# Optimization experiments

Measured on AMD Instinct MI355X. Metric: run time of the kernel, lower is better.

Reference implementation:

```python
import jax, jax.numpy as jnp
import numpy as np
from jax import lax

BOS = 0
B, T, U = 8, 256, 64
IN, ENC_H, DEC_H, P, J, V = 80, 512, 512, 512, 512, 1024


def lstm_layer(x, Wih, Whh, b):
    """PyTorch-style LSTM layer. x: [B,T,I]; Wih: [4H,I]; Whh: [4H,H]; b: [4H]."""
    Bn = x.shape[0]
    H = Whh.shape[1]
    xp = jnp.einsum('bti,gi->btg', x, Wih) + b  # precompute input projections [B,T,4H]
    h0 = jnp.zeros((Bn, H), x.dtype)

    def step(carry, xt):
        h, c = carry
        g = xt + h @ Whh.T
        i, f, gg, o = jnp.split(g, 4, axis=-1)
        c = jax.nn.sigmoid(f) * c + jax.nn.sigmoid(i) * jnp.tanh(gg)
        h = jax.nn.sigmoid(o) * jnp.tanh(c)
        return (h, c), h

    _, hs = lax.scan(step, (h0, h0), xp.transpose(1, 0, 2))
    return hs.transpose(1, 0, 2)  # [B,T,H]


def setup_inputs() -> dict:
    key = jax.random.key(0)
    ks = jax.random.split(key, 20)
    s = 0.04  # ~1/sqrt(H) init scale
    inp = {
        'xs': jax.random.normal(ks[0], (B, T, IN), jnp.float32),
        'ys': jax.random.randint(ks[1], (B, U), 0, V),
        # encoder LSTM layer 0 / 1
        'enc_Wih0': jax.random.normal(ks[2], (4 * ENC_H, IN), jnp.float32) * s,
        'enc_Whh0': jax.random.normal(ks[3], (4 * ENC_H, ENC_H), jnp.float32) * s,
        'enc_b0': jnp.zeros((4 * ENC_H,), jnp.float32),
        'enc_Wih1': jax.random.normal(ks[4], (4 * ENC_H, ENC_H), jnp.float32) * s,
        'enc_Whh1': jax.random.normal(ks[5], (4 * ENC_H, ENC_H), jnp.float32) * s,
        'enc_b1': jnp.zeros((4 * ENC_H,), jnp.float32),
        'enc_projW': jax.random.normal(ks[6], (P, ENC_H), jnp.float32) * s,
        'enc_projb': jnp.zeros((P,), jnp.float32),
        # decoder
        'embed': jax.random.normal(ks[7], (V, DEC_H), jnp.float32) * s,
        'dec_Wih': jax.random.normal(ks[8], (4 * DEC_H, DEC_H), jnp.float32) * s,
        'dec_Whh': jax.random.normal(ks[9], (4 * DEC_H, DEC_H), jnp.float32) * s,
        'dec_b': jnp.zeros((4 * DEC_H,), jnp.float32),
        'dec_projW': jax.random.normal(ks[10], (P, DEC_H), jnp.float32) * s,
        'dec_projb': jnp.zeros((P,), jnp.float32),
        # joint MLP: Linear(2P -> J), Tanh, Linear(J -> V)
        'jW1': jax.random.normal(ks[11], (J, 2 * P), jnp.float32) * s,
        'jb1': jnp.zeros((J,), jnp.float32),
        'jW2': jax.random.normal(ks[12], (V, J), jnp.float32) * s,
        'jb2': jnp.zeros((V,), jnp.float32),
    }
    return inp


def reference(xs, ys, enc_Wih0, enc_Whh0, enc_b0, enc_Wih1, enc_Whh1, enc_b1,
              enc_projW, enc_projb, embed, dec_Wih, dec_Whh, dec_b,
              dec_projW, dec_projb, jW1, jb1, jW2, jb2):
    # Encoder: 2-layer LSTM + projection
    h = lstm_layer(xs, enc_Wih0, enc_Whh0, enc_b0)
    h = lstm_layer(h, enc_Wih1, enc_Whh1, enc_b1)
    h_enc = h @ enc_projW.T + enc_projb  # [B,T,P]

    # Decoder: BOS pad, embed, 1-layer LSTM + projection
    ys_p = jnp.pad(ys, ((0, 0), (1, 0)), constant_values=BOS)  # [B,U+1]
    e = embed[ys_p]
    hd = lstm_layer(e, dec_Wih, dec_Whh, dec_b)
    h_dec = hd @ dec_projW.T + dec_projb  # [B,U+1,P]

    # Joint: cat([h_enc,h_dec]) @ W1.T == h_enc @ W1[:,:P].T + h_dec @ W1[:,P:].T
    pre_enc = jnp.einsum('btp,jp->btj', h_enc, jW1[:, :P])
    pre_dec = jnp.einsum('bup,jp->buj', h_dec, jW1[:, P:])
    z = jnp.tanh(pre_enc[:, :, None, :] + pre_dec[:, None, :, :] + jb1)  # [B,T,U+1,J]
    logits = jnp.einsum('btuj,vj->btuv', z, jW2) + jb2  # [B,T,U+1,V]
    return logits
```

## Files before the change

kernel.cpp:

```cpp
#include <hip/hip_runtime.h>


typedef _Float16 f16;
typedef _Float16 f16x8 __attribute__((ext_vector_type(8)));
typedef float f32x4 __attribute__((ext_vector_type(4)));
using u32 = unsigned int;

#define BB   8
#define TT   256
#define UU1  65
#define HH   512
#define G4   2048
#define JJ   512
#define VV   1024
#define SENT 0xFFFFFFFFu

#define LOADX(p)     __hip_atomic_load((p), __ATOMIC_RELAXED, __HIP_MEMORY_SCOPE_AGENT)
#define STOREX(p, v) __hip_atomic_store((p), (v), __ATOMIC_RELAXED, __HIP_MEMORY_SCOPE_AGENT)

static __device__ __forceinline__ u32 packf16(float a, float b) {
  f16 ha = (f16)a, hb = (f16)b;
  unsigned short ua = __builtin_bit_cast(unsigned short, ha);
  unsigned short ub = __builtin_bit_cast(unsigned short, hb);
  return (u32)ua | ((u32)ub << 16);
}
static __device__ __forceinline__ float sigm(float x) {
  x = fminf(30.f, fmaxf(-30.f, x));
  return __builtin_amdgcn_rcpf(1.f + __expf(-x));
}
static __device__ __forceinline__ float ftanh(float x) {
  x = fminf(15.f, fmaxf(-15.f, x));
  float t = __expf(2.f * x);
  return (t - 1.f) * __builtin_amdgcn_rcpf(t + 1.f);
}

__global__ void k_init(u32* __restrict__ p, int n, int z1, int z2, int zt) {
  int i = blockIdx.x * 256 + threadIdx.x;
  if (i >= n) return;
  bool z = (i < 2048) | ((u32)(i - z1) < 2048u) | ((u32)(i - z2) < 2048u) | (i >= zt);
  p[i] = z ? 0u : SENT;
}

struct CastSeg { const float* s; f16* d; int n4; };
struct CastArgs { CastSeg seg[10]; };
__global__ void k_cast_all(CastArgs a, int total4) {
  int i = blockIdx.x * 256 + threadIdx.x;
  if (i >= total4) return;
  int k = 0, off = i;
  while (off >= a.seg[k].n4) { off -= a.seg[k].n4; ++k; }
  const float4 v = *(const float4*)(a.seg[k].s + (size_t)off * 4);
  uint2 p; p.x = packf16(v.x, v.y); p.y = packf16(v.z, v.w);
  *(uint2*)(a.seg[k].d + (size_t)off * 4) = p;
}

__global__ void k_embed(const int* __restrict__ ys, const float* __restrict__ emb,
                        float* __restrict__ e) {
  int row = blockIdx.x;
  int b = row / UU1, u = row % UU1;
  int idx = (u == 0) ? 0 : ys[b * (UU1 - 1) + (u - 1)];
  const float4* s = (const float4*)(emb + (size_t)idx * HH);
  float4* d = (float4*)(e + (size_t)row * HH);
  d[threadIdx.x] = s[threadIdx.x];
}

__global__ void k_biasdot(const float* __restrict__ jW1, const float* __restrict__ encPb,
                          const float* __restrict__ dPb, const float* __restrict__ jb1,
                          float* __restrict__ bce, float* __restrict__ bcd) {
  int j = blockIdx.x * 256 + threadIdx.x;
  if (j >= 512) return;
  const float* rowE = jW1 + (size_t)j * 1024;
  const float* rowD = rowE + 512;
  float s1 = 0.f, s2 = 0.f;
  for (int p = 0; p < 512; p += 4) {
    float4 a = *(const float4*)(rowE + p), b = *(const float4*)(encPb + p);
    s1 += a.x * b.x + a.y * b.y + a.z * b.z + a.w * b.w;
    float4 c = *(const float4*)(rowD + p), d = *(const float4*)(dPb + p);
    s2 += c.x * d.x + c.y * d.y + c.z * d.z + c.w * d.w;
  }
  bce[j] = s1; bcd[j] = s2 + jb1[j];
}

__global__ __launch_bounds__(256) void k_gemm(
    const float* __restrict__ A, const f16* __restrict__ B,
    const float* __restrict__ bias, float* __restrict__ C,
    int M, int N, int K, int lda, int ldb) {
  __shared__ f16 As[128][72];
  __shared__ f16 Bs[128][72];
  int tid = threadIdx.x;
  int mb = blockIdx.y * 128, nb = blockIdx.x * 128;
  int wave = tid >> 6, lane = tid & 63;
  int wm = wave >> 1, wn = wave & 1;
  int rowa = lane & 15, kg = lane >> 4;
  f32x4 acc[4][4] = {};
  for (int k0 = 0; k0 < K; k0 += 64) {
    for (int idx = tid; idx < 2048; idx += 256) {
      int r = idx >> 4, cq = idx & 15;
      int gm = mb + r, gk = k0 + cq * 4;
      float4 v = make_float4(0.f, 0.f, 0.f, 0.f);
      if (gm < M && gk + 3 < K) v = *(const float4*)(A + (size_t)gm * lda + gk);
      uint2 p; p.x = packf16(v.x, v.y); p.y = packf16(v.z, v.w);
      *(uint2*)&As[r][cq * 4] = p;
    }
    for (int idx = tid; idx < 1024; idx += 256) {
      int r = idx >> 3, c8 = idx & 7;
      int gn = nb + r, gk = k0 + c8 * 8;
      uint4 v = make_uint4(0u, 0u, 0u, 0u);
      if (gn < N && gk + 7 < K) v = *(const uint4*)(B + (size_t)gn * ldb + gk);
      *(uint4*)&Bs[r][c8 * 8] = v;
    }
    __syncthreads();
#pragma unroll
    for (int kf = 0; kf < 2; ++kf) {
      f16x8 af[4], bf[4];
#pragma unroll
      for (int mt = 0; mt < 4; ++mt)
        af[mt] = *(const f16x8*)&As[wm * 64 + mt * 16 + rowa][kf * 32 + kg * 8];
#pragma unroll
      for (int nt = 0; nt < 4; ++nt)
        bf[nt] = *(const f16x8*)&Bs[wn * 64 + nt * 16 + rowa][kf * 32 + kg * 8];
#pragma unroll
      for (int mt = 0; mt < 4; ++mt)
#pragma unroll
        for (int nt = 0; nt < 4; ++nt)
          acc[mt][nt] = __builtin_amdgcn_mfma_f32_16x16x32_f16(af[mt], bf[nt], acc[mt][nt], 0, 0, 0);
    }
    __syncthreads();
  }
#pragma unroll
  for (int nt = 0; nt < 4; ++nt) {
    int gn = nb + wn * 64 + nt * 16 + rowa;
    float bv = bias ? bias[gn] : 0.f;
#pragma unroll
    for (int mt = 0; mt < 4; ++mt)
#pragma unroll
      for (int r = 0; r < 4; ++r) {
        int gm = mb + wm * 64 + mt * 16 + kg * 4 + r;
        if (gm < M) C[(size_t)gm * N + gn] = acc[mt][nt][r] + bv;
      }
  }
}

__global__ __launch_bounds__(256) void k_gemmT(
    const float* __restrict__ A, int lda, const f16* __restrict__ B2,
    f16* __restrict__ C16) {
  __shared__ f16 As[128][72];
  __shared__ f16 Bs[128][72];
  int tid = threadIdx.x;
  int mb = blockIdx.y * 128, nb = blockIdx.x * 128;
  int wave = tid >> 6, lane = tid & 63;
  int wm = wave >> 1, wn = wave & 1;
  int rowa = lane & 15, kg = lane >> 4;
  f32x4 acc[4][4] = {};
  for (int k0 = 0; k0 < 512; k0 += 64) {
    for (int idx = tid; idx < 2048; idx += 256) {
      int r = idx >> 4, cq = idx & 15;
      float4 v = *(const float4*)(A + (size_t)(mb + r) * lda + k0 + cq * 4);
      uint2 p; p.x = packf16(v.x, v.y); p.y = packf16(v.z, v.w);
      *(uint2*)&As[r][cq * 4] = p;
    }
    for (int idx = tid; idx < 1024; idx += 256) {
      int r = idx >> 4, c8 = idx & 15;
      uint4 v = *(const uint4*)(B2 + (size_t)(k0 + r) * 512 + nb + c8 * 8);
      f16 tmp[8]; *(uint4*)tmp = v;
#pragma unroll
      for (int e = 0; e < 8; ++e) Bs[c8 * 8 + e][r] = tmp[e];
    }
    __syncthreads();
#pragma unroll
    for (int kf = 0; kf < 2; ++kf) {
      f16x8 af[4], bf[4];
#pragma unroll
      for (int mt = 0; mt < 4; ++mt)
        af[mt] = *(const f16x8*)&As[wm * 64 + mt * 16 + rowa][kf * 32 + kg * 8];
#pragma unroll
      for (int nt = 0; nt < 4; ++nt)
        bf[nt] = *(const f16x8*)&Bs[wn * 64 + nt * 16 + rowa][kf * 32 + kg * 8];
#pragma unroll
      for (int mt = 0; mt < 4; ++mt)
#pragma unroll
        for (int nt = 0; nt < 4; ++nt)
          acc[mt][nt] = __builtin_amdgcn_mfma_f32_16x16x32_f16(af[mt], bf[nt], acc[mt][nt], 0, 0, 0);
    }
    __syncthreads();
  }
#pragma unroll
  for (int nt = 0; nt < 4; ++nt) {
    int gn = nb + wn * 64 + nt * 16 + rowa;
#pragma unroll
    for (int mt = 0; mt < 4; ++mt)
#pragma unroll
      for (int r = 0; r < 4; ++r) {
        int gm = mb + wm * 64 + mt * 16 + kg * 4 + r;
        C16[(size_t)gm * 512 + gn] = (f16)acc[mt][nt][r];
      }
  }
}

template <int NW>
static __device__ __forceinline__ void poll_batch(const u32* const* p, u32* vv) {
#pragma unroll
  for (int k = 0; k < NW; ++k) vv[k] = LOADX(p[k]);
  int gd = 0;
  while (++gd < (1 << 18)) {
    bool any = false;
#pragma unroll
    for (int k = 0; k < NW; ++k) any = any | (vv[k] == SENT);
    if (!any) break;
    __builtin_amdgcn_s_sleep(4);
#pragma unroll
    for (int k = 0; k < NW; ++k)
      if (vv[k] == SENT) vv[k] = LOADX(p[k]);
  }
}
static __device__ __forceinline__ void guard_spin(const u32* gp) {
  u32 v = LOADX(gp);
  int gd = 0;
  while (v == SENT && ++gd < (1 << 18)) {
    __builtin_amdgcn_s_sleep(1);
    v = LOADX(gp);
  }
}
static __device__ __forceinline__ void prog_spin(const u32* fp) {
  u32 v = LOADX(fp);
  int gd = 0;
  while (v < 8u && ++gd < (1 << 18)) {
    __builtin_amdgcn_s_sleep(8);
    v = LOADX(fp);
  }
}

static __device__ __forceinline__ void lstm_16(
    int wg, const float* __restrict__ xp, const f16* __restrict__ Whh,
    u32* __restrict__ hseq, int S) {
  extern __shared__ char smem[];
  f16 (*W)[520] = (f16(*)[520])smem;
  f16 (*H)[520] = (f16(*)[520])(smem + 133120);
  float (*gat)[8][36] = (float(*)[8][36])(smem + 133120 + 8320);
  const int tid = threadIdx.x;
  const int u0 = wg * 32;
  const int wave = tid >> 6, lane = tid & 63;
  const int rowa = lane & 15, kg = lane >> 4;
  const int b = lane >> 3, ju = lane & 7;
  const int uglob = u0 + wave * 8 + ju;

  for (int idx = tid; idx < 128 * 64; idx += 256) {
    int r = idx >> 6, ck = idx & 63;
    int w = r >> 5, g = (r >> 3) & 3, u = r & 7;
    uint4 v = *(const uint4*)(Whh + ((size_t)(g * 512 + u0 + w * 8 + u)) * 512 + ck * 8);
    *(uint4*)&W[r][ck * 8] = v;
  }
  __syncthreads();

  float c = 0.f;
  for (int t = 0; t < S; ++t) {
    const u32* hb = hseq + (size_t)t * 2048;
    if (tid < 16) guard_spin(hb + tid * 16);
    __syncthreads();

    size_t xpo = ((size_t)b * S + t) * (size_t)G4 + uglob;
    float xi = xp[xpo], xf = xp[xpo + 512], xg = xp[xpo + 1024], xo = xp[xpo + 1536];

    const u32* ptr[8];
    u32 vv[8];
#pragma unroll
    for (int k = 0; k < 8; ++k) ptr[k] = hb + ((tid + k * 256) >> 8) * 256 + ((tid + k * 256) & 255);
    poll_batch<8>(ptr, vv);
#pragma unroll
    for (int k = 0; k < 8; ++k) {
      int idx = tid + k * 256;
      ((u32*)H)[(idx >> 8) * 260 + (idx & 255)] = vv[k];
    }
    __syncthreads();

    f32x4 acc0 = {0.f, 0.f, 0.f, 0.f}, acc1 = {0.f, 0.f, 0.f, 0.f};
#pragma unroll
    for (int kf = 0; kf < 16; ++kf) {
      f16x8 af = {};
      if (rowa < 8) af = *(const f16x8*)&H[rowa][kf * 32 + kg * 8];
      f16x8 b0 = *(const f16x8*)&W[wave * 32 + rowa][kf * 32 + kg * 8];
      f16x8 b1 = *(const f16x8*)&W[wave * 32 + 16 + rowa][kf * 32 + kg * 8];
      acc0 = __builtin_amdgcn_mfma_f32_16x16x32_f16(af, b0, acc0, 0, 0, 0);
      acc1 = __builtin_amdgcn_mfma_f32_16x16x32_f16(af, b1, acc1, 0, 0, 0);
    }
    if (kg < 2) {
#pragma unroll
      for (int r = 0; r < 4; ++r) {
        gat[wave][kg * 4 + r][rowa] = acc0[r];
        gat[wave][kg * 4 + r][16 + rowa] = acc1[r];
      }
    }
    float gi = gat[wave][b][ju] + xi;
    float gf = gat[wave][b][8 + ju] + xf;
    float gg = gat[wave][b][16 + ju] + xg;
    float go = gat[wave][b][24 + ju] + xo;
    c = sigm(gf) * c + sigm(gi) * ftanh(gg);
    float h = sigm(go) * ftanh(c);

    float hn = __shfl_down(h, 1);
    if ((ju & 1) == 0)
      STOREX(hseq + (size_t)(t + 1) * 2048 + ((b * 512 + uglob) >> 1), packf16(h, hn));
  }
}

static __device__ __forceinline__ void lstm_l1(
    int wg, const float* __restrict__ gb, const f16* __restrict__ Wih,
    const f16* __restrict__ Whh, const u32* __restrict__ hin,
    u32* __restrict__ hseq, int S) {
  extern __shared__ char smem[];
  f16 (*W)[1032] = (f16(*)[1032])smem;
  f16 (*H)[1032] = (f16(*)[1032])(smem + 132096);
  float (*gat)[8][20] = (float(*)[8][20])(smem + 132096 + 16512);
  const int tid = threadIdx.x;
  const int u0 = wg * 16;
  const int wave = tid >> 6, lane = tid & 63;
  const int rowa = lane & 15, kg = lane >> 4;
  const int b = lane >> 2, ju = lane & 3;
  const int uglob = u0 + wave * 4 + ju;

  for (int idx = tid; idx < 64 * 64; idx += 256) {
    int r = idx >> 6, ck = idx & 63;
    int w = r >> 4, g = (r >> 2) & 3, u = r & 3;
    size_t grow = (size_t)(g * 512 + u0 + w * 4 + u) * 512;
    *(uint4*)&W[r][ck * 8]       = *(const uint4*)(Whh + grow + ck * 8);
    *(uint4*)&W[r][512 + ck * 8] = *(const uint4*)(Wih + grow + ck * 8);
  }
  float gbi = 0.f, gbf = 0.f, gbg = 0.f, gbo = 0.f;
  if (lane < 32) {
    gbi = gb[uglob]; gbf = gb[512 + uglob];
    gbg = gb[1024 + uglob]; gbo = gb[1536 + uglob];
  }
  __syncthreads();

  float c = 0.f;
  for (int t = 0; t < S; ++t) {
    const u32* hbS = hseq + (size_t)t * 2048;
    const u32* hbU = hin + (size_t)(t + 1) * 2048;
    if (tid < 32)       guard_spin(hbS + tid * 8);
    else if (tid < 48)  guard_spin(hbU + (tid - 32) * 16);
    __syncthreads();
    const u32* ptr[16];
    u32 vv[16];
#pragma unroll
    for (int k = 0; k < 8; ++k) {
      int idx = tid + k * 256;
      int r = idx >> 8, cu = idx & 255;
      ptr[k] = hbS + r * 256 + cu;
      ptr[k + 8] = hbU + r * 256 + cu;
    }
    poll_batch<16>(ptr, vv);
#pragma unroll
    for (int k = 0; k < 8; ++k) {
      int idx = tid + k * 256;
      int r = idx >> 8, cu = idx & 255;
      ((u32*)H)[r * 516 + cu] = vv[k];
      ((u32*)H)[r * 516 + 256 + cu] = vv[k + 8];
    }
    __syncthreads();

    f32x4 accA = {0.f, 0.f, 0.f, 0.f}, accB = {0.f, 0.f, 0.f, 0.f};
#pragma unroll
    for (int kf = 0; kf < 16; ++kf) {
      f16x8 afA = {}, afB = {};
      if (rowa < 8) {
        afA = *(const f16x8*)&H[rowa][kf * 32 + kg * 8];
        afB = *(const f16x8*)&H[rowa][(kf + 16) * 32 + kg * 8];
      }
      f16x8 bfA = *(const f16x8*)&W[wave * 16 + rowa][kf * 32 + kg * 8];
      f16x8 bfB = *(const f16x8*)&W[wave * 16 + rowa][(kf + 16) * 32 + kg * 8];
      accA = __builtin_amdgcn_mfma_f32_16x16x32_f16(afA, bfA, accA, 0, 0, 0);
      accB = __builtin_amdgcn_mfma_f32_16x16x32_f16(afB, bfB, accB, 0, 0, 0);
    }
    if (kg < 2) {
#pragma unroll
      for (int r = 0; r < 4; ++r) gat[wave][kg * 4 + r][rowa] = accA[r] + accB[r];
    }
    if (lane < 32) {
      float gi = gat[wave][b][ju]      + gbi;
      float gf = gat[wave][b][4 + ju]  + gbf;
      float gg = gat[wave][b][8 + ju]  + gbg;
      float go = gat[wave][b][12 + ju] + gbo;
      c = sigm(gf) * c + sigm(gi) * ftanh(gg);
      float h = sigm(go) * ftanh(c);
      float hn = __shfl_down(h, 1);
      if ((ju & 1) == 0)
        STOREX(hseq + (size_t)(t + 1) * 2048 + (b * 256 + (uglob >> 1)), packf16(h, hn));
    }
  }
}

static __device__ __forceinline__ void proj_prod(
    int wg, const u32* __restrict__ hseq, const f16* __restrict__ Wc,
    const float* __restrict__ bc, float* __restrict__ outS,
    u32* __restrict__ prog, int S, int gs, int gc) {
  extern __shared__ char smem[];
  f16 (*W)[520] = (f16(*)[520])smem;
  f16 (*H)[520] = (f16(*)[520])(smem + 66560);
  const int tid = threadIdx.x;
  const int wave = tid >> 6, lane = tid & 63;
  const int rowa = lane & 15, kg = lane >> 4;
  const int c0 = wg * 64;
  const int j = c0 + wave * 16 + rowa;

  for (int idx = tid; idx < 64 * 64; idx += 256) {
    int r = idx >> 6, ck = idx & 63;
    uint4 v = *(const uint4*)(Wc + (size_t)(c0 + r) * 512 + ck * 8);
    *(uint4*)&W[r][ck * 8] = v;
  }
  for (int idx = tid; idx < 16 * 260; idx += 256) ((u32*)H)[idx] = 0u;
  const float bj = bc[j];
  __syncthreads();

  for (int t = 0; t < S; ++t) {
    const u32* hb = hseq + (size_t)(t + 1) * 2048;
    if (tid < gc) guard_spin(hb + tid * gs);
    __syncthreads();
    const u32* ptr[8];
    u32 vv[8];
#pragma unroll
    for (int k = 0; k < 8; ++k) ptr[k] = hb + ((tid + k * 256) >> 8) * 256 + ((tid + k * 256) & 255);
    poll_batch<8>(ptr, vv);
#pragma unroll
    for (int k = 0; k < 8; ++k) {
      int idx = tid + k * 256;
      ((u32*)H)[(idx >> 8) * 260 + (idx & 255)] = vv[k];
    }
    __syncthreads();

    f32x4 acc = {0.f, 0.f, 0.f, 0.f};
#pragma unroll
    for (int kf = 0; kf < 16; ++kf) {
      f16x8 af = {};
      if (rowa < 8) af = *(const f16x8*)&H[rowa][kf * 32 + kg * 8];
      f16x8 bf = *(const f16x8*)&W[wave * 16 + rowa][kf * 32 + kg * 8];
      acc = __builtin_amdgcn_mfma_f32_16x16x32_f16(af, bf, acc, 0, 0, 0);
    }
    if (kg < 2) {
#pragma unroll
      for (int r = 0; r < 4; ++r) {
        float val = acc[r] + bj;
        STOREX((u32*)(outS + ((size_t)t * 8 + kg * 4 + r) * 512 + j),
               __builtin_bit_cast(u32, val));
      }
    }
    __syncthreads();
    if (tid == 0)
      __hip_atomic_fetch_add(prog + t, 1u, __ATOMIC_RELAXED, __HIP_MEMORY_SCOPE_AGENT);
  }
}

static __device__ __forceinline__ void joint_tile(
    int j, const float* __restrict__ pencS, const float* __restrict__ pdecS,
    const u32* __restrict__ pencProg, const u32* __restrict__ pdecProg,
    const f16* __restrict__ jW2, const float* __restrict__ jb2,
    float* __restrict__ out) {
  extern __shared__ char smem[];
  f16 (*Z)[520] = (f16(*)[520])smem;
  f16 (*Bs)[72] = (f16(*)[72])(smem + 49920);
  float (*Cs)[68] = (float(*)[68])(smem + 49920 + 9216);
  const int tid = threadIdx.x;
  const int t = j >> 4, b = (j >> 1) & 7, uh = j & 1;
  const int u0 = uh * 32, nrow = uh ? 33 : 32;
  const size_t mbase = (size_t)b * (TT * UU1) + (size_t)t * UU1 + u0;
  const int wave = tid >> 6, lane = tid & 63;
  const int rowa = lane & 15, kg = lane >> 4;

  const int rr = tid >> 2, cc = (tid & 3) * 16;
  uint4 n0 = *(const uint4*)(jW2 + (size_t)rr * JJ + cc);
  uint4 n1 = *(const uint4*)(jW2 + (size_t)rr * JJ + cc + 8);

  for (int idx = tid; idx < 48 * 260; idx += 256) ((u32*)Z)[idx] = 0u;

  if (tid == 0) prog_spin(pencProg + t);
  else if (tid >= 64 && tid < 64 + nrow) prog_spin(pdecProg + u0 + (tid - 64));
  __syncthreads();

  {
    const float* pe = pencS + ((size_t)t * 8 + b) * 512;
    for (int r = tid >> 4; r < nrow; r += 16) {
      const float* pd = pdecS + ((size_t)(u0 + r) * 8 + b) * 512;
      int cbase = (tid & 15) * 32;
      for (int c8 = 0; c8 < 4; ++c8) {
        float ve[8], vd[8];
#pragma unroll
        for (int k = 0; k < 8; ++k) {
          ve[k] = __builtin_bit_cast(float, LOADX((const u32*)(pe + cbase + c8 * 8 + k)));
          vd[k] = __builtin_bit_cast(float, LOADX((const u32*)(pd + cbase + c8 * 8 + k)));
        }
        uint4 p;
        p.x = packf16(ftanh(ve[0] + vd[0]), ftanh(ve[1] + vd[1]));
        p.y = packf16(ftanh(ve[2] + vd[2]), ftanh(ve[3] + vd[3]));
        p.z = packf16(ftanh(ve[4] + vd[4]), ftanh(ve[5] + vd[5]));
        p.w = packf16(ftanh(ve[6] + vd[6]), ftanh(ve[7] + vd[7]));
        *(uint4*)&Z[r][cbase + c8 * 8] = p;
      }
    }
  }

  f32x4 acc[3] = {};
  for (int it = 0; it < 128; ++it) {
    const int vc = it >> 3, ks = it & 7;
    __syncthreads();
    *(uint4*)&Bs[rr][cc] = n0;
    *(uint4*)&Bs[rr][cc + 8] = n1;
    if (it < 127) {
      int nvc = (it + 1) >> 3, nks = (it + 1) & 7;
      const f16* p = jW2 + (size_t)(nvc * 64 + rr) * JJ + nks * 64 + cc;
      n0 = *(const uint4*)p;
      n1 = *(const uint4*)(p + 8);
    }
    __syncthreads();
#pragma unroll
    for (int kf = 0; kf < 2; ++kf) {
      f16x8 af = *(const f16x8*)&Bs[wave * 16 + rowa][kf * 32 + kg * 8];
#pragma unroll
      for (int mt = 0; mt < 3; ++mt) {
        f16x8 bf = *(const f16x8*)&Z[mt * 16 + rowa][ks * 64 + kf * 32 + kg * 8];
        acc[mt] = __builtin_amdgcn_mfma_f32_16x16x32_f16(af, bf, acc[mt], 0, 0, 0);
      }
    }
    if (ks == 7) {
      int vl = wave * 16 + kg * 4;
      float4 bv = *(const float4*)(jb2 + vc * 64 + vl);
#pragma unroll
      for (int mt = 0; mt < 3; ++mt) {
        int row = mt * 16 + rowa;
        if (row < nrow) {
          f32x4 st;
          st[0] = acc[mt][0] + bv.x; st[1] = acc[mt][1] + bv.y;
          st[2] = acc[mt][2] + bv.z; st[3] = acc[mt][3] + bv.w;
          *(f32x4*)&Cs[row][vl] = st;
        }
        acc[mt] = (f32x4){0.f, 0.f, 0.f, 0.f};
      }
      __syncthreads();
      for (int r = tid >> 4; r < nrow; r += 16) {
        int vi = (tid & 15) * 4;
        f32x4 rowv = *(const f32x4*)&Cs[r][vi];
        __builtin_nontemporal_store(rowv,
            (f32x4*)(out + (mbase + r) * VV + vc * 64 + vi));
      }
    }
  }
}

__global__ __launch_bounds__(256, 1) void k_all(
    const float* xp0, const f16* Whh0, u32* hseq0,
    const float* b1, const f16* Wih1, const f16* Whh1, u32* hseq1,
    const float* xpd, const f16* Whhd, u32* hseqD,
    const f16* Wce, const float* bce, float* pencS, u32* pencProg,
    const f16* Wcd, const float* bcd, float* pdecS, u32* pdecProg,
    const f16* jW2, const float* jb2, float* out) {
  int g = blockIdx.x;
  if (g < 16)       lstm_16(g, xp0, Whh0, hseq0, TT);
  else if (g < 48)  lstm_l1(g - 16, b1, Wih1, Whh1, hseq0, hseq1, TT);
  else if (g < 64)  lstm_16(g - 48, xpd, Whhd, hseqD, UU1);
  else if (g < 72)  proj_prod(g - 64, hseq1, Wce, bce, pencS, pencProg, TT, 8, 32);
  else if (g < 80)  proj_prod(g - 72, hseqD, Wcd, bcd, pdecS, pdecProg, UU1, 16, 16);
  else              joint_tile(g - 80, pencS, pdecS, pencProg, pdecProg, jW2, jb2, out);
}

extern "C" void kernel_launch(void* const* d_in, const int* in_sizes, int n_in,
                              void* d_out, int out_size, void* d_ws, size_t ws_size,
                              hipStream_t stream) {
  const float* xs    = (const float*)d_in[0];
  const int*   ys    = (const int*)d_in[1];
  const float* Wih0  = (const float*)d_in[2];
  const float* Whh0  = (const float*)d_in[3];
  const float* b0    = (const float*)d_in[4];
  const float* Wih1  = (const float*)d_in[5];
  const float* Whh1  = (const float*)d_in[6];
  const float* b1    = (const float*)d_in[7];
  const float* encPW = (const float*)d_in[8];
  const float* encPb = (const float*)d_in[9];
  const float* embed = (const float*)d_in[10];
  const float* dWih  = (const float*)d_in[11];
  const float* dWhh  = (const float*)d_in[12];
  const float* db    = (const float*)d_in[13];
  const float* dPW   = (const float*)d_in[14];
  const float* dPb   = (const float*)d_in[15];
  const float* jW1   = (const float*)d_in[16];
  const float* jb1   = (const float*)d_in[17];
  const float* jW2   = (const float*)d_in[18];
  const float* jb2   = (const float*)d_in[19];
  float* out = (float*)d_out;

  char* base = (char*)d_ws;
  size_t off = 0;
  auto alc = [&](size_t bytes) -> char* {
    char* p = base + off;
    off = (off + bytes + 255) & ~(size_t)255;
    return p;
  };
  f16* Wih0h = (f16*)alc((size_t)2048 * 80 * 2);
  f16* Whh0h = (f16*)alc((size_t)2048 * 512 * 2);
  f16* Wih1h = (f16*)alc((size_t)2048 * 512 * 2);
  f16* Whh1h = (f16*)alc((size_t)2048 * 512 * 2);
  f16* dWihh = (f16*)alc((size_t)2048 * 512 * 2);
  f16* dWhhh = (f16*)alc((size_t)2048 * 512 * 2);
  f16* ePWh  = (f16*)alc((size_t)512 * 512 * 2);
  f16* dPWh  = (f16*)alc((size_t)512 * 512 * 2);
  f16* jW2h  = (f16*)alc((size_t)1024 * 512 * 2);
  f16* Wceh  = (f16*)alc((size_t)512 * 512 * 2);
  f16* Wcdh  = (f16*)alc((size_t)512 * 512 * 2);
  float* bce  = (float*)alc((size_t)512 * 4);
  float* bcd  = (float*)alc((size_t)512 * 4);
  float* e    = (float*)alc((size_t)520 * 512 * 4);
  float* xp0  = (float*)alc((size_t)2048 * 2048 * 4);
  float* xpd  = (float*)alc((size_t)520 * 2048 * 4);
  u32* hseq0 = (u32*)alc((size_t)(TT + 1) * 2048 * 4);
  u32* hseq1 = (u32*)alc((size_t)(TT + 1) * 2048 * 4);
  u32* hseqD = (u32*)alc((size_t)(UU1 + 1) * 2048 * 4);
  float* pencS = (float*)alc((size_t)TT * 8 * 512 * 4);
  float* pdecS = (float*)alc((size_t)UU1 * 8 * 512 * 4);
  u32* pencProg = (u32*)alc((size_t)TT * 4);
  u32* pdecProg = (u32*)alc((size_t)UU1 * 4);
  if (off > ws_size) return;

  {
    int n = (int)((pdecProg + UU1) - hseq0);
    int z1 = (int)(hseq1 - hseq0), z2 = (int)(hseqD - hseq0);
    int zt = (int)(pencProg - hseq0);
    k_init<<<dim3((n + 255) / 256), dim3(256), 0, stream>>>(hseq0, n, z1, z2, zt);
  }
  {
    CastArgs ca = {};
    auto seg = [&](int i, const float* s, f16* d, size_t n) {
      ca.seg[i].s = s; ca.seg[i].d = d; ca.seg[i].n4 = (int)(n / 4);
    };
    seg(0, Wih0, Wih0h, (size_t)2048 * 80);
    seg(1, Whh0, Whh0h, (size_t)2048 * 512);
    seg(2, Wih1, Wih1h, (size_t)2048 * 512);
    seg(3, Whh1, Whh1h, (size_t)2048 * 512);
    seg(4, dWih, dWihh, (size_t)2048 * 512);
    seg(5, dWhh, dWhhh, (size_t)2048 * 512);
    seg(6, encPW, ePWh, (size_t)512 * 512);
    seg(7, dPW, dPWh, (size_t)512 * 512);
    seg(8, jW2, jW2h, (size_t)1024 * 512);
    int total4 = 0;
    for (int i = 0; i < 9; ++i) total4 += ca.seg[i].n4;
    k_cast_all<<<dim3((total4 + 255) / 256), dim3(256), 0, stream>>>(ca, total4);
  }
  k_gemmT<<<dim3(4, 4), dim3(256), 0, stream>>>(jW1, 1024, ePWh, Wceh);
  k_gemmT<<<dim3(4, 4), dim3(256), 0, stream>>>(jW1 + 512, 1024, dPWh, Wcdh);
  k_biasdot<<<dim3(2), dim3(256), 0, stream>>>(jW1, encPb, dPb, jb1, bce, bcd);

  k_embed<<<dim3(520), dim3(128), 0, stream>>>(ys, embed, e);

  auto gemm = [&](const float* A, const f16* B, const float* bias, float* C,
                  int M, int N, int K, int lda, int ldb) {
    k_gemm<<<dim3(N / 128, (M + 127) / 128), dim3(256), 0, stream>>>(
        A, B, bias, C, M, N, K, lda, ldb);
  };

  gemm(xs, Wih0h, b0, xp0, 2048, 2048, 80, 80, 80);
  gemm(e, dWihh, db, xpd, 520, 2048, 512, 512, 512);

  k_all<<<dim3(80 + 4096), dim3(256), 151168, stream>>>(
      xp0, Whh0h, hseq0,
      b1, Wih1h, Whh1h, hseq1,
      xpd, dWhhh, hseqD,
      Wceh, bce, pencS, pencProg,
      Wcdh, bcd, pdecS, pdecProg,
      jW2h, jb2, out);
}
```

Baseline: 1.684 ms.

## Stage full-K jW2 tiles in LDS per vocab chunk to cut barriers

The joint tile now loads a whole 64x512 slice of jW2 into shared memory for each 64-column vocab chunk, instead of a 64x64 slice per K step. The 8 K steps per chunk are fully unrolled, so there are 2 barriers per chunk instead of 2 per K step. The next chunk is prefetched into 16 uint4 registers per thread. In exchange, shared memory use grows by about 57 KB and register pressure rises, which may limit occupancy. The host-side dynamic shared memory size must also match the larger footprint.

```diff
diff --git a/kernel.cpp b/kernel.cpp
--- a/kernel.cpp
+++ b/kernel.cpp
@@ -455,8 +455,8 @@
     float* __restrict__ out) {
   extern __shared__ char smem[];
   f16 (*Z)[520] = (f16(*)[520])smem;
-  f16 (*Bs)[72] = (f16(*)[72])(smem + 49920);
-  float (*Cs)[68] = (float(*)[68])(smem + 49920 + 9216);
+  f16 (*Bs)[520] = (f16(*)[520])(smem + 49920);
+  float (*Cs)[68] = (float(*)[68])(smem + 49920 + 66560);
   const int tid = threadIdx.x;
   const int t = j >> 4, b = (j >> 1) & 7, uh = j & 1;
   const int u0 = uh * 32, nrow = uh ? 33 : 32;
@@ -464,9 +464,12 @@
   const int wave = tid >> 6, lane = tid & 63;
   const int rowa = lane & 15, kg = lane >> 4;
 
-  const int rr = tid >> 2, cc = (tid & 3) * 16;
-  uint4 n0 = *(const uint4*)(jW2 + (size_t)rr * JJ + cc);
-  uint4 n1 = *(const uint4*)(jW2 + (size_t)rr * JJ + cc + 8);
+  const int br = tid >> 2, bc = (tid & 3) * 128;
+
+  uint4 pb[16];
+#pragma unroll
+  for (int k = 0; k < 16; ++k)
+    pb[k] = *(const uint4*)(jW2 + (size_t)br * JJ + bc + k * 8);
 
   for (int idx = tid; idx < 48 * 260; idx += 256) ((u32*)Z)[idx] = 0u;
 
@@ -496,49 +499,47 @@
     }
   }
 
-  f32x4 acc[3] = {};
-  for (int it = 0; it < 128; ++it) {
-    const int vc = it >> 3, ks = it & 7;
-    __syncthreads();
-    *(uint4*)&Bs[rr][cc] = n0;
-    *(uint4*)&Bs[rr][cc + 8] = n1;
-    if (it < 127) {
-      int nvc = (it + 1) >> 3, nks = (it + 1) & 7;
-      const f16* p = jW2 + (size_t)(nvc * 64 + rr) * JJ + nks * 64 + cc;
-      n0 = *(const uint4*)p;
-      n1 = *(const uint4*)(p + 8);
-    }
-    __syncthreads();
-#pragma unroll
-    for (int kf = 0; kf < 2; ++kf) {
-      f16x8 af = *(const f16x8*)&Bs[wave * 16 + rowa][kf * 32 + kg * 8];
-#pragma unroll
-      for (int mt = 0; mt < 3; ++mt) {
-        f16x8 bf = *(const f16x8*)&Z[mt * 16 + rowa][ks * 64 + kf * 32 + kg * 8];
-        acc[mt] = __builtin_amdgcn_mfma_f32_16x16x32_f16(af, bf, acc[mt], 0, 0, 0);
-      }
-    }
-    if (ks == 7) {
-      int vl = wave * 16 + kg * 4;
-      float4 bv = *(const float4*)(jb2 + vc * 64 + vl);
-#pragma unroll
-      for (int mt = 0; mt < 3; ++mt) {
-        int row = mt * 16 + rowa;
-        if (row < nrow) {
-          f32x4 st;
-          st[0] = acc[mt][0] + bv.x; st[1] = acc[mt][1] + bv.y;
-          st[2] = acc[mt][2] + bv.z; st[3] = acc[mt][3] + bv.w;
-          *(f32x4*)&Cs[row][vl] = st;
+  for (int vc = 0; vc < 16; ++vc) {
+    __syncthreads();
+#pragma unroll
+    for (int k = 0; k < 16; ++k) *(uint4*)&Bs[br][bc + k * 8] = pb[k];
+    __syncthreads();
+    if (vc < 15) {
+#pragma unroll
+      for (int k = 0; k < 16; ++k)
+        pb[k] = *(const uint4*)(jW2 + (size_t)((vc + 1) * 64 + br) * JJ + bc + k * 8);
+    }
+    f32x4 acc[3] = {};
+#pragma unroll
+    for (int ks = 0; ks < 8; ++ks)
+#pragma unroll
+      for (int kf = 0; kf < 2; ++kf) {
+        int co = ks * 64 + kf * 32 + kg * 8;
+        f16x8 af = *(const f16x8*)&Bs[wave * 16 + rowa][co];
+#pragma unroll
+        for (int mt = 0; mt < 3; ++mt) {
+          f16x8 bf = *(const f16x8*)&Z[mt * 16 + rowa][co];
+          acc[mt] = __builtin_amdgcn_mfma_f32_16x16x32_f16(af, bf, acc[mt], 0, 0, 0);
         }
-        acc[mt] = (f32x4){0.f, 0.f, 0.f, 0.f};
-      }
-      __syncthreads();
-      for (int r = tid >> 4; r < nrow; r += 16) {
-        int vi = (tid & 15) * 4;
-        f32x4 rowv = *(const f32x4*)&Cs[r][vi];
-        __builtin_nontemporal_store(rowv,
-            (f32x4*)(out + (mbase + r) * VV + vc * 64 + vi));
-      }
+      }
+    int vl = wave * 16 + kg * 4;
+    float4 bv = *(const float4*)(jb2 + vc * 64 + vl);
+#pragma unroll
+    for (int mt = 0; mt < 3; ++mt) {
+      int row = mt * 16 + rowa;
+      if (row < nrow) {
+        f32x4 st;
+        st[0] = acc[mt][0] + bv.x; st[1] = acc[mt][1] + bv.y;
+        st[2] = acc[mt][2] + bv.z; st[3] = acc[mt][3] + bv.w;
+        *(f32x4*)&Cs[row][vl] = st;
+      }
+    }
+    __syncthreads();
+    for (int r = tid >> 4; r < nrow; r += 16) {
+      int vi = (tid & 15) * 4;
+      f32x4 rowv = *(const f32x4*)&Cs[r][vi];
+      __builtin_nontemporal_store(rowv,
+          (f32x4*)(out + (mbase + r) * VV + vc * 64 + vi));
     }
   }
 }
```

After: 2.630 ms. 1.56x slower.
